# Kernel optimization log

Measured on AMD Instinct MI355X. Metric: run time of the kernel, lower is better.

## Reference

```python
import jax, jax.numpy as jnp
import numpy as np

# Standard 4-level FPN pyramid for an ~800x1200 input (RT-DETR-like)
SHAPES = [(100, 150), (50, 75), (25, 38), (13, 19)]


def setup_inputs() -> dict:
    key = jax.random.key(0)
    k1, k2, k3 = jax.random.split(key, 3)
    B, Hd, C, P = 2, 8, 32, 4
    shapes = np.array(SHAPES, dtype=np.int64)          # [Levels, 2]
    areas = shapes.prod(axis=1)
    L = int(areas.sum())                                # 19947 total tokens
    Q = L                                               # encoder self-attention
    lsi = np.concatenate([[0], np.cumsum(areas)[:-1]]).astype(np.int64)
    value = jax.random.normal(k1, (B, L, Hd, C), dtype=jnp.float32)
    sampling_locations = jax.random.uniform(k2, (B, Q, Hd, len(SHAPES), P, 2), dtype=jnp.float32)
    w = jax.random.uniform(k3, (B, Q, Hd, len(SHAPES), P), dtype=jnp.float32)
    attention_weights = w / w.sum(axis=(3, 4), keepdims=True)  # softmax-like normalization over levels*points
    return {
        "value": value,
        "spatial_shapes": jnp.asarray(shapes),
        "level_start_index": jnp.asarray(lsi),
        "sampling_locations": sampling_locations,
        "attention_weights": attention_weights,
    }


def _bilinear_sample(vflat, Hh, Ww, loc):
    """Zero-padded bilinear sampling matching the CUDA ms_deform_attn kernel.
    vflat: [BH, Hh*Ww, C]; loc: [BH, Q, P, 2] normalized to [0,1].
    Returns [BH, Q, P, C].
    """
    x = loc[..., 0] * Ww - 0.5
    y = loc[..., 1] * Hh - 0.5
    x0 = jnp.floor(x)
    y0 = jnp.floor(y)
    dx = x - x0
    dy = y - y0
    x0i = x0.astype(jnp.int32)
    y0i = y0.astype(jnp.int32)
    BH, Qn, P = x0i.shape
    out = jnp.zeros(vflat.shape[:1] + (Qn, P, vflat.shape[-1]), vflat.dtype)
    corners = [
        (y0i,     x0i,     (1 - dy) * (1 - dx)),
        (y0i,     x0i + 1, (1 - dy) * dx),
        (y0i + 1, x0i,     dy * (1 - dx)),
        (y0i + 1, x0i + 1, dy * dx),
    ]
    for yi, xi, wgt in corners:
        valid = ((yi >= 0) & (yi < Hh) & (xi >= 0) & (xi < Ww)).astype(vflat.dtype)
        idx = jnp.clip(yi, 0, Hh - 1) * Ww + jnp.clip(xi, 0, Ww - 1)  # [BH,Q,P]
        g = jnp.take_along_axis(vflat, idx.reshape(BH, Qn * P, 1), axis=1)
        g = g.reshape(BH, Qn, P, -1)
        out = out + g * (wgt * valid)[..., None]
    return out


def reference(value, spatial_shapes, level_start_index, sampling_locations, attention_weights):
    shapes = np.asarray(spatial_shapes)        # static level shapes
    starts = np.asarray(level_start_index)
    B, L, Hd, C = value.shape
    Q = sampling_locations.shape[1]
    n_levels = shapes.shape[0]
    P = sampling_locations.shape[4]
    out = jnp.zeros((B * Hd, Q, C), value.dtype)
    for l in range(n_levels):
        Hh, Ww = int(shapes[l, 0]), int(shapes[l, 1])
        s = int(starts[l])
        v = value[:, s:s + Hh * Ww]                                   # [B, HW, Hd, C]
        vflat = v.transpose(0, 2, 1, 3).reshape(B * Hd, Hh * Ww, C)   # [BH, HW, C]
        loc = sampling_locations[:, :, :, l].transpose(0, 2, 1, 3, 4).reshape(B * Hd, Q, P, 2)
        aw = attention_weights[:, :, :, l].transpose(0, 2, 1, 3).reshape(B * Hd, Q, P)
        samp = _bilinear_sample(vflat, Hh, Ww, loc)                    # [BH, Q, P, C]
        out = out + (samp * aw[..., None]).sum(axis=2)
    return out.reshape(B, Hd, Q, C).transpose(0, 2, 1, 3).reshape(B, Q, Hd * C)
```

## Files before the change

### kernel.cpp

```cpp
#include <hip/hip_runtime.h>

#define NLV  4
#define NPT  4
#define CCH  32
#define HD   8
#define QTOT 19947
#define LTOT 19947
#define BB   2

#define GPB  32
#define JOBS (GPB * 16)
#define BLOCKS_PER_SLICE ((QTOT + GPB - 1) / GPB)
#define NSLICES (BB * HD)

typedef float        f32x4 __attribute__((ext_vector_type(4)));
typedef float        f32x2 __attribute__((ext_vector_type(2)));
typedef unsigned int u32;
typedef u32          u32x4 __attribute__((ext_vector_type(4)));

__device__ __forceinline__ unsigned jslot(int gl, int s) {
    return (unsigned)((gl * 16 + (s ^ (gl & 7))) * 4);
}
#define LDS_WORDS (JOBS * 4)

__global__ __launch_bounds__(256) void msda_fwd(
    const float* __restrict__ value,
    const float* __restrict__ loc,
    const float* __restrict__ attw,
    float* __restrict__ out)
{
    __shared__ __align__(16) u32   s_ofs[LDS_WORDS];
    __shared__ __align__(16) float s_wts[LDS_WORDS];

    const int Hs[NLV] = {100, 50, 25, 13};
    const int Ws[NLV] = {150, 75, 38, 19};
    const int Ss[NLV] = {0, 15000, 18750, 19700};

    const int slice = blockIdx.x & 15;
    const int blk   = blockIdx.x >> 4;
    const int b = slice >> 3;
    const int h = slice & 7;
    const int t = (int)threadIdx.x;

#pragma unroll
    for (int jj = 0; jj < 2; ++jj) {
        const int j  = t + jj * 256;
        const int gl = j >> 4;
        const int s  = j & 15;
        const int l  = s >> 2;
        const int q  = blk * GPB + gl;
        const int qc = min(q, QTOT - 1);
        const size_t og = ((size_t)b * QTOT + qc) * HD + h;

        const f32x2 lxy = __builtin_nontemporal_load((const f32x2*)loc + og * 16 + s);
        float wa = __builtin_nontemporal_load(attw + og * 16 + s);
        if (q >= QTOT) wa = 0.f;

        const int H = Hs[l], W = Ws[l];
        const float x = lxy.x * (float)W - 0.5f;
        const float y = lxy.y * (float)H - 0.5f;
        const float x0f = floorf(x), y0f = floorf(y);
        const float dx = x - x0f,  dy = y - y0f;
        const int x0 = (int)x0f,   y0 = (int)y0f;
        const int x1 = x0 + 1,     y1 = y0 + 1;

        const bool vx0 = (x0 >= 0) & (x0 < W);
        const bool vx1 = (x1 >= 0) & (x1 < W);
        const bool vy0 = (y0 >= 0) & (y0 < H);
        const bool vy1 = (y1 >= 0) & (y1 < H);

        float w00 = (1.f - dy) * (1.f - dx) * wa;
        float w01 = (1.f - dy) * dx         * wa;
        float w10 = dy         * (1.f - dx) * wa;
        float w11 = dy         * dx         * wa;
        w00 = (vy0 & vx0) ? w00 : 0.f;
        w01 = (vy0 & vx1) ? w01 : 0.f;
        w10 = (vy1 & vx0) ? w10 : 0.f;
        w11 = (vy1 & vx1) ? w11 : 0.f;

        const int cx0 = min(max(x0, 0), W - 1);
        const int cx1 = min(max(x1, 0), W - 1);
        const int cy0 = min(max(y0, 0), H - 1);
        const int cy1 = min(max(y1, 0), H - 1);

        const u32 base = (u32)(((b * LTOT + Ss[l]) * HD + h) * CCH) * 4u;
        const u32 r0 = (u32)(cy0 * W), r1 = (u32)(cy1 * W);
        u32x4 offs;
        offs.x = base + (r0 + (u32)cx0) * (HD * CCH * 4u);
        offs.y = base + (r0 + (u32)cx1) * (HD * CCH * 4u);
        offs.z = base + (r1 + (u32)cx0) * (HD * CCH * 4u);
        offs.w = base + (r1 + (u32)cx1) * (HD * CCH * 4u);
        f32x4 wts;
        wts.x = w00; wts.y = w01; wts.z = w10; wts.w = w11;

        const unsigned sb = jslot(gl, s);
        *(u32x4*)&s_ofs[sb] = offs;
        *(f32x4*)&s_wts[sb] = wts;
    }

    __syncthreads();

    const int gl   = t >> 3;
    const int lane = t & 7;
    const int q    = blk * GPB + gl;
    const char* vb = (const char*)value + lane * 16;

    f32x4 acc = {0.f, 0.f, 0.f, 0.f};
#pragma unroll
    for (int s = 0; s < 16; ++s) {
        const unsigned sb = jslot(gl, s);
        const u32x4 offs = *(const u32x4*)&s_ofs[sb];
        const f32x4 w    = *(const f32x4*)&s_wts[sb];
        const f32x4 g0 = *(const f32x4*)(vb + offs.x);
        const f32x4 g1 = *(const f32x4*)(vb + offs.y);
        const f32x4 g2 = *(const f32x4*)(vb + offs.z);
        const f32x4 g3 = *(const f32x4*)(vb + offs.w);
        acc += g0 * w.x;
        acc += g1 * w.y;
        acc += g2 * w.z;
        acc += g3 * w.w;
    }

    if (q < QTOT) {
        const size_t og = ((size_t)b * QTOT + q) * HD + h;
        __builtin_nontemporal_store(acc, (f32x4*)out + og * 8 + lane);
    }
}

extern "C" void kernel_launch(void* const* d_in, const int* in_sizes, int n_in,
                              void* d_out, int out_size, void* d_ws, size_t ws_size,
                              hipStream_t stream) {
    const float* value = (const float*)d_in[0];
    const float* loc   = (const float*)d_in[3];
    const float* attw  = (const float*)d_in[4];
    float* out = (float*)d_out;

    msda_fwd<<<BLOCKS_PER_SLICE * NSLICES, 256, 0, stream>>>(value, loc, attw, out);
}
```

Measured before the change: 239.1 us.

## Convert value tensor to fp16 in workspace before bilinear gather

Adds a pre-pass that converts the fp32 value tensor into fp16 in the workspace. The main kernel then gathers 16-byte fp16 chunks (8 channels per lane, 4 lanes per query) and handles 64 queries per block, with a wider LDS swizzle. The aim is to halve the gather bytes and the cache footprint of the random bilinear reads. The cost is an extra conversion pass over the whole value tensor and fp16 rounding of the inputs. An fp32 fallback path is kept for when the workspace is too small.

Result: slower. 266.1 us (+11.3%).

```diff
diff --git a/kernel.cpp b/kernel.cpp
--- a/kernel.cpp
+++ b/kernel.cpp
@@ -1,30 +1,48 @@
 #include <hip/hip_runtime.h>
 
 #define NLV  4
-#define NPT  4
 #define CCH  32
 #define HD   8
 #define QTOT 19947
 #define LTOT 19947
 #define BB   2
 
-#define GPB  32
+typedef float        f32x4 __attribute__((ext_vector_type(4)));
+typedef float        f32x2 __attribute__((ext_vector_type(2)));
+typedef _Float16     f16x8 __attribute__((ext_vector_type(8)));
+typedef unsigned int u32;
+typedef u32          u32x4 __attribute__((ext_vector_type(4)));
+
+#define VAL16_ELEMS (BB * LTOT * HD * CCH)
+#define VAL16_BYTES (VAL16_ELEMS * 2)
+
+__global__ __launch_bounds__(256) void cvt_value_f16(
+    const float* __restrict__ value, _Float16* __restrict__ v16)
+{
+    const int i = blockIdx.x * 256 + (int)threadIdx.x;
+    if (i >= VAL16_ELEMS / 8) return;
+    const f32x4 a = ((const f32x4*)value)[i * 2 + 0];
+    const f32x4 b = ((const f32x4*)value)[i * 2 + 1];
+    f16x8 o;
+    o[0] = (_Float16)a.x; o[1] = (_Float16)a.y;
+    o[2] = (_Float16)a.z; o[3] = (_Float16)a.w;
+    o[4] = (_Float16)b.x; o[5] = (_Float16)b.y;
+    o[6] = (_Float16)b.z; o[7] = (_Float16)b.w;
+    ((f16x8*)v16)[i] = o;
+}
+
+#define GPB  64
 #define JOBS (GPB * 16)
 #define BLOCKS_PER_SLICE ((QTOT + GPB - 1) / GPB)
 #define NSLICES (BB * HD)
 
-typedef float        f32x4 __attribute__((ext_vector_type(4)));
-typedef float        f32x2 __attribute__((ext_vector_type(2)));
-typedef unsigned int u32;
-typedef u32          u32x4 __attribute__((ext_vector_type(4)));
-
-__device__ __forceinline__ unsigned jslot(int gl, int s) {
-    return (unsigned)((gl * 16 + (s ^ (gl & 7))) * 4);
+__device__ __forceinline__ unsigned jslot16(int gl, int s) {
+    return (unsigned)((gl * 16 + (s ^ (gl & 15))) * 4);
 }
 #define LDS_WORDS (JOBS * 4)
 
-__global__ __launch_bounds__(256) void msda_fwd(
-    const float* __restrict__ value,
+__global__ __launch_bounds__(256) void msda_fwd_f16(
+    const _Float16* __restrict__ v16,
     const float* __restrict__ loc,
     const float* __restrict__ attw,
     float* __restrict__ out)
@@ -43,7 +61,7 @@
     const int t = (int)threadIdx.x;
 
 #pragma unroll
-    for (int jj = 0; jj < 2; ++jj) {
+    for (int jj = 0; jj < 4; ++jj) {
         const int j  = t + jj * 256;
         const int gl = j >> 4;
         const int s  = j & 15;
@@ -83,6 +101,101 @@
         const int cy0 = min(max(y0, 0), H - 1);
         const int cy1 = min(max(y1, 0), H - 1);
 
+        const u32 base = (u32)(((b * LTOT + Ss[l]) * HD + h) * (CCH * 2));
+        const u32 r0 = (u32)(cy0 * W), r1 = (u32)(cy1 * W);
+        u32x4 offs;
+        offs.x = base + (r0 + (u32)cx0) * (HD * CCH * 2u);
+        offs.y = base + (r0 + (u32)cx1) * (HD * CCH * 2u);
+        offs.z = base + (r1 + (u32)cx0) * (HD * CCH * 2u);
+        offs.w = base + (r1 + (u32)cx1) * (HD * CCH * 2u);
+        f32x4 wts;
+        wts.x = w00; wts.y = w01; wts.z = w10; wts.w = w11;
+
+        const unsigned sb = jslot16(gl, s);
+        *(u32x4*)&s_ofs[sb] = offs;
+        *(f32x4*)&s_wts[sb] = wts;
+    }
+
+    __syncthreads();
+
+    const int gl   = t >> 2;
+    const int lane = t & 3;
+    const int q    = blk * GPB + gl;
+    const char* vb = (const char*)v16 + lane * 16;
+
+    float acc[8] = {0.f, 0.f, 0.f, 0.f, 0.f, 0.f, 0.f, 0.f};
+#pragma unroll
+    for (int s = 0; s < 16; ++s) {
+        const unsigned sb = jslot16(gl, s);
+        const u32x4 offs = *(const u32x4*)&s_ofs[sb];
+        const f32x4 w    = *(const f32x4*)&s_wts[sb];
+        const f16x8 g0 = *(const f16x8*)(vb + offs.x);
+        const f16x8 g1 = *(const f16x8*)(vb + offs.y);
+        const f16x8 g2 = *(const f16x8*)(vb + offs.z);
+        const f16x8 g3 = *(const f16x8*)(vb + offs.w);
+#pragma unroll
+        for (int c = 0; c < 8; ++c) {
+            acc[c] += (float)g0[c] * w.x;
+            acc[c] += (float)g1[c] * w.y;
+            acc[c] += (float)g2[c] * w.z;
+            acc[c] += (float)g3[c] * w.w;
+        }
+    }
+
+    if (q < QTOT) {
+        const size_t og = ((size_t)b * QTOT + q) * HD + h;
+        f32x4 lo, hi;
+        lo.x = acc[0]; lo.y = acc[1]; lo.z = acc[2]; lo.w = acc[3];
+        hi.x = acc[4]; hi.y = acc[5]; hi.z = acc[6]; hi.w = acc[7];
+        __builtin_nontemporal_store(lo, (f32x4*)out + og * 8 + lane * 2);
+        __builtin_nontemporal_store(hi, (f32x4*)out + og * 8 + lane * 2 + 1);
+    }
+}
+
+#define FGPB 32
+#define FJOBS (FGPB * 16)
+__device__ __forceinline__ unsigned fjslot(int gl, int s) {
+    return (unsigned)((gl * 16 + (s ^ (gl & 7))) * 4);
+}
+__global__ __launch_bounds__(256) void msda_fwd_f32(
+    const float* __restrict__ value,
+    const float* __restrict__ loc,
+    const float* __restrict__ attw,
+    float* __restrict__ out)
+{
+    __shared__ __align__(16) u32   s_ofs[FJOBS * 4];
+    __shared__ __align__(16) float s_wts[FJOBS * 4];
+    const int Hs[NLV] = {100, 50, 25, 13};
+    const int Ws[NLV] = {150, 75, 38, 19};
+    const int Ss[NLV] = {0, 15000, 18750, 19700};
+    const int slice = blockIdx.x & 15;
+    const int blk   = blockIdx.x >> 4;
+    const int b = slice >> 3, h = slice & 7;
+    const int t = (int)threadIdx.x;
+#pragma unroll
+    for (int jj = 0; jj < 2; ++jj) {
+        const int j  = t + jj * 256;
+        const int gl = j >> 4, s = j & 15, l = s >> 2;
+        const int q  = blk * FGPB + gl;
+        const int qc = min(q, QTOT - 1);
+        const size_t og = ((size_t)b * QTOT + qc) * HD + h;
+        const f32x2 lxy = __builtin_nontemporal_load((const f32x2*)loc + og * 16 + s);
+        float wa = __builtin_nontemporal_load(attw + og * 16 + s);
+        if (q >= QTOT) wa = 0.f;
+        const int H = Hs[l], W = Ws[l];
+        const float x = lxy.x * (float)W - 0.5f;
+        const float y = lxy.y * (float)H - 0.5f;
+        const float x0f = floorf(x), y0f = floorf(y);
+        const float dx = x - x0f, dy = y - y0f;
+        const int x0 = (int)x0f, y0 = (int)y0f, x1 = x0 + 1, y1 = y0 + 1;
+        const bool vx0 = (x0 >= 0) & (x0 < W), vx1 = (x1 >= 0) & (x1 < W);
+        const bool vy0 = (y0 >= 0) & (y0 < H), vy1 = (y1 >= 0) & (y1 < H);
+        float w00 = (1.f - dy) * (1.f - dx) * wa, w01 = (1.f - dy) * dx * wa;
+        float w10 = dy * (1.f - dx) * wa,         w11 = dy * dx * wa;
+        w00 = (vy0 & vx0) ? w00 : 0.f; w01 = (vy0 & vx1) ? w01 : 0.f;
+        w10 = (vy1 & vx0) ? w10 : 0.f; w11 = (vy1 & vx1) ? w11 : 0.f;
+        const int cx0 = min(max(x0, 0), W - 1), cx1 = min(max(x1, 0), W - 1);
+        const int cy0 = min(max(y0, 0), H - 1), cy1 = min(max(y1, 0), H - 1);
         const u32 base = (u32)(((b * LTOT + Ss[l]) * HD + h) * CCH) * 4u;
         const u32 r0 = (u32)(cy0 * W), r1 = (u32)(cy1 * W);
         u32x4 offs;
@@ -90,37 +203,26 @@
         offs.y = base + (r0 + (u32)cx1) * (HD * CCH * 4u);
         offs.z = base + (r1 + (u32)cx0) * (HD * CCH * 4u);
         offs.w = base + (r1 + (u32)cx1) * (HD * CCH * 4u);
-        f32x4 wts;
-        wts.x = w00; wts.y = w01; wts.z = w10; wts.w = w11;
-
-        const unsigned sb = jslot(gl, s);
+        f32x4 wts; wts.x = w00; wts.y = w01; wts.z = w10; wts.w = w11;
+        const unsigned sb = fjslot(gl, s);
         *(u32x4*)&s_ofs[sb] = offs;
         *(f32x4*)&s_wts[sb] = wts;
     }
-
     __syncthreads();
-
-    const int gl   = t >> 3;
-    const int lane = t & 7;
-    const int q    = blk * GPB + gl;
+    const int gl = t >> 3, lane = t & 7;
+    const int q  = blk * FGPB + gl;
     const char* vb = (const char*)value + lane * 16;
-
     f32x4 acc = {0.f, 0.f, 0.f, 0.f};
 #pragma unroll
     for (int s = 0; s < 16; ++s) {
-        const unsigned sb = jslot(gl, s);
+        const unsigned sb = fjslot(gl, s);
         const u32x4 offs = *(const u32x4*)&s_ofs[sb];
         const f32x4 w    = *(const f32x4*)&s_wts[sb];
-        const f32x4 g0 = *(const f32x4*)(vb + offs.x);
-        const f32x4 g1 = *(const f32x4*)(vb + offs.y);
-        const f32x4 g2 = *(const f32x4*)(vb + offs.z);
-        const f32x4 g3 = *(const f32x4*)(vb + offs.w);
-        acc += g0 * w.x;
-        acc += g1 * w.y;
-        acc += g2 * w.z;
-        acc += g3 * w.w;
-    }
-
+        acc += (*(const f32x4*)(vb + offs.x)) * w.x;
+        acc += (*(const f32x4*)(vb + offs.y)) * w.y;
+        acc += (*(const f32x4*)(vb + offs.z)) * w.z;
+        acc += (*(const f32x4*)(vb + offs.w)) * w.w;
+    }
     if (q < QTOT) {
         const size_t og = ((size_t)b * QTOT + q) * HD + h;
         __builtin_nontemporal_store(acc, (f32x4*)out + og * 8 + lane);
@@ -135,5 +237,11 @@
     const float* attw  = (const float*)d_in[4];
     float* out = (float*)d_out;
 
-    msda_fwd<<<BLOCKS_PER_SLICE * NSLICES, 256, 0, stream>>>(value, loc, attw, out);
-}
+    if (ws_size >= (size_t)VAL16_BYTES) {
+        _Float16* v16 = (_Float16*)d_ws;
+        cvt_value_f16<<<(VAL16_ELEMS / 8 + 255) / 256, 256, 0, stream>>>(value, v16);
+        msda_fwd_f16<<<BLOCKS_PER_SLICE * NSLICES, 256, 0, stream>>>(v16, loc, attw, out);
+    } else {
+        msda_fwd_f32<<<((QTOT + FGPB - 1) / FGPB) * NSLICES, 256, 0, stream>>>(value, loc, attw, out);
+    }
+}
```
